# Performance work log

Hardware: AMD Instinct MI355X
Metric: run time of the kernel (lower is better)

## Reference

```python
import jax, jax.numpy as jnp
import numpy as np

B, C, H, W = 8, 512, 32, 32
N = H * W
FG_THRES, BG_THRES, TOPK = 0.7, 0.6, 12


def setup_inputs() -> dict:
    key = jax.random.key(0)
    k1, k2, k3 = jax.random.split(key, 3)
    feature_q = jax.random.normal(k1, (B, C, H, W), dtype=jnp.float32)
    support_feat = jax.random.normal(k2, (B, C, H, W), dtype=jnp.float32)
    support_mask = jax.random.randint(k3, (B, H, W), 0, 2).astype(jnp.int32)
    return {"feature_q": feature_q, "support_feat": support_feat, "support_mask": support_mask}


def _masked_avg_pool(feat, mask):
    # feat [B,C,H,W], mask [B,1,H,W]; interpolate to same size is identity
    return jnp.sum(feat * mask, axis=(2, 3)) / (jnp.sum(mask, axis=(2, 3)) + 1e-5)


def _cosine(a, b):
    # F.cosine_similarity along channel dim 1 (eps=1e-8), with broadcasting
    dot = jnp.sum(a * b, axis=1)
    na = jnp.sqrt(jnp.sum(a * a, axis=1))
    nb = jnp.sqrt(jnp.sum(b * b, axis=1))
    return dot / jnp.maximum(na * nb, 1e-8)


def _similarity(feature_q, fg_proto, bg_proto):
    sim_fg = _cosine(feature_q, fg_proto)
    sim_bg = _cosine(feature_q, bg_proto)
    return jnp.stack([sim_bg, sim_fg], axis=1) * 10.0  # [B,2,H,W]


def _select_weights(pred, thres):
    # pred [N] -> float {0,1} selection weights; threshold mask, topk-12 fallback
    m = pred > thres
    _, top_idx = jax.lax.top_k(pred, TOPK)
    tm = jnp.zeros_like(m).at[top_idx].set(True)
    return jnp.where(m.sum() > 0, m, tm).astype(pred.dtype)


def _ssp_single(cur_feat, pred_fg, pred_bg):
    # cur_feat [C,N]; masked formulation == torch's variable-length column select
    wf = _select_weights(pred_fg, FG_THRES)
    wb = _select_weights(pred_bg, BG_THRES)
    fg_proto = jnp.sum(cur_feat * wf, axis=-1) / wf.sum()  # [C]
    bg_proto = jnp.sum(cur_feat * wb, axis=-1) / wb.sum()
    cn = cur_feat / jnp.sqrt(jnp.sum(cur_feat * cur_feat, axis=0, keepdims=True))
    sim = (cn.T @ cn) * 2.0  # [N,N] cosine sim, scaled
    neg = jnp.asarray(-1e30, sim.dtype)
    fg_attn = jax.nn.softmax(jnp.where(wf[None, :] > 0, sim, neg), axis=-1)
    bg_attn = jax.nn.softmax(jnp.where(wb[None, :] > 0, sim, neg), axis=-1)
    fg_local = (fg_attn @ cur_feat.T).T  # [C,N]
    bg_local = (bg_attn @ cur_feat.T).T
    return fg_proto, bg_proto, fg_local, bg_local


def reference(feature_q, support_feat, support_mask):
    mask_f = (support_mask == 1).astype(feature_q.dtype)[:, None]  # [B,1,H,W]
    mask_b = (support_mask == 0).astype(feature_q.dtype)[:, None]
    FP = _masked_avg_pool(support_feat, mask_f)[:, :, None, None]  # [B,C,1,1]
    BP = _masked_avg_pool(support_feat, mask_b)[:, :, None, None]
    out_0 = _similarity(feature_q, FP, BP)  # [B,2,H,W]
    pred = jax.nn.softmax(out_0, axis=1).reshape(B, 2, N)
    cur = feature_q.reshape(B, C, N)
    fg_p, bg_p, fg_l, bg_l = jax.vmap(_ssp_single)(cur, pred[:, 1], pred[:, 0])
    SSFP = fg_p[:, :, None, None]
    SSBP = bg_p[:, :, None, None]
    ASBP = bg_l.reshape(B, C, H, W)
    FP_1 = FP * 0.5 + SSFP * 0.5
    BP_1 = SSBP * 0.3 + ASBP * 0.7
    out_1 = _similarity(feature_q, FP_1, BP_1)  # [B,2,H,W]
    return out_1
```

## Files before the change

### kernel.cpp

```cpp
#include <hip/hip_runtime.h>
#include <math.h>

#define Bsz 8
#define Cch 512
#define Npx 1024
#define TOPK 12
#define BN (Bsz * Npx)

typedef __attribute__((ext_vector_type(8))) short bf16x8;
typedef __attribute__((ext_vector_type(4))) float f32x4;

__device__ __forceinline__ unsigned short f2bf(float x) {
    unsigned u = __float_as_uint(x);
    u += 0x7FFF + ((u >> 16) & 1);
    return (unsigned short)(u >> 16);
}
__device__ __forceinline__ float bf2f(unsigned short h) {
    return __uint_as_float(((unsigned)h) << 16);
}

__device__ __forceinline__ float warp_sum64(float v) {
    for (int o = 32; o > 0; o >>= 1) v += __shfl_down(v, o);
    return v;
}
__device__ __forceinline__ float block_sum512(float v, float* s8) {
    v = warp_sum64(v);
    int lane = threadIdx.x & 63, w = threadIdx.x >> 6;
    __syncthreads();
    if (lane == 0) s8[w] = v;
    __syncthreads();
    float r = 0.f;
    #pragma unroll
    for (int k = 0; k < 8; k++) r += s8[k];
    return r;
}

__global__ void k_pool(const float* __restrict__ sf, const int* __restrict__ mask,
                       float* __restrict__ FPo, float* __restrict__ BPo) {
    __shared__ float s4a[4], s4b[4], s4c[4];
    int c = blockIdx.x, b = blockIdx.y, t = threadIdx.x;
    const float4* f4 = (const float4*)(sf + ((size_t)b * Cch + c) * Npx);
    const int4* m4 = (const int4*)(mask + (size_t)b * Npx);
    float4 v = f4[t];
    int4 m = m4[t];
    float sumf = (m.x == 1 ? v.x : 0.f) + (m.y == 1 ? v.y : 0.f)
               + (m.z == 1 ? v.z : 0.f) + (m.w == 1 ? v.w : 0.f);
    float tot = v.x + v.y + v.z + v.w;
    float cf = (float)((m.x == 1) + (m.y == 1) + (m.z == 1) + (m.w == 1));
    sumf = warp_sum64(sumf);
    tot  = warp_sum64(tot);
    cf   = warp_sum64(cf);
    int lane = t & 63, w = t >> 6;
    if (lane == 0) { s4a[w] = sumf; s4b[w] = tot; s4c[w] = cf; }
    __syncthreads();
    if (t == 0) {
        float sA = s4a[0] + s4a[1] + s4a[2] + s4a[3];
        float sB = s4b[0] + s4b[1] + s4b[2] + s4b[3];
        float sC = s4c[0] + s4c[1] + s4c[2] + s4c[3];
        FPo[b * Cch + c] = sA / (sC + 1e-5f);
        BPo[b * Cch + c] = (sB - sA) / ((1024.f - sC) + 1e-5f);
    }
}

__global__ void __launch_bounds__(512) k_predcast(const float* __restrict__ fq,
                       const float* __restrict__ FP, const float* __restrict__ BP,
                       float* __restrict__ dsim, float* __restrict__ invn,
                       unsigned short* __restrict__ Ft) {
    __shared__ float sFP[Cch], sBP[Cch], s8[8];
    __shared__ float rdf[16][32], rdb[16][32], rqq[16][32];
    __shared__ unsigned short S[32][522];
    int b = blockIdx.y, t = threadIdx.x;
    int tx = t & 31, ty = t >> 5;
    int p0 = blockIdx.x * 32;
    int p = p0 + tx;
    sFP[t] = FP[b * Cch + t];
    sBP[t] = BP[b * Cch + t];
    __syncthreads();
    float nf = sqrtf(block_sum512(sFP[t] * sFP[t], s8));
    float nb = sqrtf(block_sum512(sBP[t] * sBP[t], s8));
    const float* q = fq + (size_t)b * Cch * Npx + p;
    float df = 0.f, db = 0.f, qq = 0.f;
    int c0 = ty * 32;
    #pragma unroll 4
    for (int c = 0; c < 32; c += 2) {
        float v0 = q[(size_t)(c0 + c) * Npx];
        float v1 = q[(size_t)(c0 + c + 1) * Npx];
        df += v0 * sFP[c0 + c] + v1 * sFP[c0 + c + 1];
        db += v0 * sBP[c0 + c] + v1 * sBP[c0 + c + 1];
        qq += v0 * v0 + v1 * v1;
        unsigned pk = (unsigned)f2bf(v0) | ((unsigned)f2bf(v1) << 16);
        *(unsigned*)&S[tx][c0 + c] = pk;
    }
    rdf[ty][tx] = df; rdb[ty][tx] = db; rqq[ty][tx] = qq;
    __syncthreads();
    for (int s = 8; s > 0; s >>= 1) {
        if (ty < s) {
            rdf[ty][tx] += rdf[ty + s][tx];
            rdb[ty][tx] += rdb[ty + s][tx];
            rqq[ty][tx] += rqq[ty + s][tx];
        }
        __syncthreads();
    }
    if (ty == 0) {
        float nq = sqrtf(rqq[0][tx]);
        float simf = 10.f * rdf[0][tx] / fmaxf(nq * nf, 1e-8f);
        float simb = 10.f * rdb[0][tx] / fmaxf(nq * nb, 1e-8f);
        dsim[b * Npx + p] = simf - simb;
        invn[b * Npx + p] = 1.f / nq;
    }
    int w = t >> 6, lane = t & 63;
    unsigned short* FtB = Ft + (size_t)b * Npx * Cch;
    for (int pr = w; pr < 32; pr += 8) {
        unsigned* dst = (unsigned*)(FtB + (size_t)(p0 + pr) * Cch);
        #pragma unroll
        for (int it = 0; it < 4; it++) {
            int d = it * 64 + lane;
            dst[d] = *(const unsigned*)&S[pr][d * 2];
        }
    }
}

__global__ void __launch_bounds__(1024) k_selcompact(const float* __restrict__ dsim,
                        const float* __restrict__ invn,
                        const unsigned short* __restrict__ Ft,
                        const float* __restrict__ FP,
                        int* __restrict__ nsf, int* __restrict__ nsb,
                        int* __restrict__ jf, int* __restrict__ jb,
                        float* __restrict__ ivg,
                        float* __restrict__ fgp, float* __restrict__ bgp,
                        float* __restrict__ FP1, float* __restrict__ nfv) {
    __shared__ int wsum[16];
    __shared__ int sns;
    __shared__ float sProto[16][512];
    __shared__ float s16f[16];
    int b = blockIdx.y, t = threadIdx.x;
    int lane = t & 63, w = t >> 6;
    bool isf = (blockIdx.x == 0);
    float d = dsim[b * Npx + t];
    float key = isf ? d : -d;
    float thres = isf ? 0.8472979f : 0.4054651f;
    int flag = (key > thres) ? 1 : 0;
    int x = flag;
    #pragma unroll
    for (int o = 1; o < 64; o <<= 1) {
        int y = __shfl_up(x, o);
        if (lane >= o) x += y;
    }
    if (lane == 63) wsum[w] = x;
    __syncthreads();
    int base = 0, total = 0;
    #pragma unroll
    for (int k = 0; k < 16; k++) {
        int s = wsum[k];
        if (k < w) base += s;
        total += s;
    }
    int* jdst = (isf ? jf : jb) + b * Npx;
    if (total == 0) {
        __shared__ int   sc[Npx];
        __shared__ float v[Npx];
        __shared__ float rv[Npx];
        __shared__ int   ri[Npx];
        v[t] = key; flag = 0;
        __syncthreads();
        for (int k = 0; k < TOPK; k++) {
            rv[t] = v[t]; ri[t] = t;
            __syncthreads();
            for (int s = 512; s > 0; s >>= 1) {
                if (t < s) {
                    float a = rv[t], bb = rv[t + s];
                    int ia = ri[t], ib = ri[t + s];
                    if (bb > a || (bb == a && ib < ia)) { rv[t] = bb; ri[t] = ib; }
                }
                __syncthreads();
            }
            int win = ri[0];
            if (t == win) { flag = 1; v[t] = -INFINITY; }
            __syncthreads();
        }
        sc[t] = flag;
        __syncthreads();
        for (int off = 1; off < 1024; off <<= 1) {
            int xx = (t >= off) ? sc[t - off] : 0;
            __syncthreads();
            sc[t] += xx;
            __syncthreads();
        }
        if (flag) {
            int pos = sc[t] - 1;
            jdst[pos] = t;
            if (!isf) ivg[b * Npx + pos] = invn[b * Npx + t];
        }
        if (t == 1023) sns = sc[1023];
    } else {
        if (flag) {
            int pos = base + x - 1;
            jdst[pos] = t;
            if (!isf) ivg[b * Npx + pos] = invn[b * Npx + t];
        }
        if (t == 0) sns = total;
    }
    __syncthreads();
    int ns = sns;
    if (t == 0) (isf ? nsf : nsb)[b] = ns;
    const unsigned short* FtB = Ft + (size_t)b * Npx * Cch;
    float facc[8] = {0.f, 0.f, 0.f, 0.f, 0.f, 0.f, 0.f, 0.f};
    int k = w;
    int row = (k < ns) ? jdst[k] : 0;
    while (k < ns) {
        int kn = k + 16;
        int rown = (kn < ns) ? jdst[kn] : 0;
        bf16x8 vv = *(const bf16x8*)&FtB[(size_t)row * Cch + lane * 8];
        #pragma unroll
        for (int e = 0; e < 8; e++) facc[e] += bf2f((unsigned short)vv[e]);
        k = kn; row = rown;
    }
    #pragma unroll
    for (int e = 0; e < 8; e++) sProto[w][lane * 8 + e] = facc[e];
    __syncthreads();
    float fp1 = 0.f;
    if (t < 512) {
        float s = 0.f;
        #pragma unroll
        for (int q = 0; q < 16; q++) s += sProto[q][t];
        float pv = s / (float)ns;
        (isf ? fgp : bgp)[b * Cch + t] = pv;
        if (isf) {
            fp1 = 0.5f * FP[b * Cch + t] + 0.5f * pv;
            FP1[b * Cch + t] = fp1;
        }
    }
    if (isf) {
        float v2 = warp_sum64(fp1 * fp1);
        if (lane == 0) s16f[w] = v2;
        __syncthreads();
        if (t == 0) {
            float nn = 0.f;
            #pragma unroll
            for (int q = 0; q < 16; q++) nn += s16f[q];
            nfv[b] = sqrtf(nn);
        }
    }
}

__global__ void __launch_bounds__(512) k_fused(
        const unsigned short* __restrict__ Ft,
        const int* __restrict__ jb, const int* __restrict__ nsb,
        const float* __restrict__ invn, const float* __restrict__ ivg,
        const float* __restrict__ bgp, const float* __restrict__ FP1,
        const float* __restrict__ nfv, float* __restrict__ out) {
    __shared__ unsigned short U[36864];
    __shared__ unsigned short sP[32][1032];
    __shared__ int   sji[1024];
    __shared__ float sfj[1024];
    __shared__ float sfp1full[Cch], sbgfull[Cch];
    __shared__ float sfi[32], sden[32];
    __shared__ float spart[32][3];

    unsigned short (*Bt2)[64][136] = (unsigned short(*)[64][136])U;
    unsigned short (*Vt)[72] = (unsigned short(*)[72])U;

    int bid = blockIdx.x;
    int b = bid & 7;
    int i0 = (bid >> 3) * 32;
    int tid = threadIdx.x;
    int l = tid & 63, w = tid >> 6;
    int ml = l & 15, quad = l >> 4;
    int ns = nsb[b];
    int K64 = ((((ns + 31) & ~31) + 63) & ~63);
    int T = K64 >> 6;

    const unsigned short* FtB = Ft + (size_t)b * Npx * Cch;
    int ig = w & 1, jg = w >> 1;

    bf16x8 afr[4][4];
    {
        const unsigned short* aro = FtB + (size_t)(i0 + ig * 16 + ml) * Cch + quad * 8;
        #pragma unroll
        for (int kt = 0; kt < 4; kt++)
            #pragma unroll
            for (int h = 0; h < 4; h++)
                afr[kt][h] = *(const bf16x8*)(aro + kt * 128 + h * 32);
    }

    for (int j = tid; j < K64; j += 512) {
        sji[j] = (j < ns) ? jb[b * Npx + j] : jb[b * Npx];
        sfj[j] = (j < ns) ? ivg[b * Npx + j] : 0.f;
    }
    sfp1full[tid] = FP1[b * Cch + tid];
    sbgfull[tid]  = 0.3f * bgp[b * Cch + tid];
    if (tid < 32) sfi[tid] = 2.f * invn[b * Npx + i0 + tid];
    __syncthreads();

    int grow = tid >> 4, gk8 = (tid & 15) * 8;
    for (int j0 = 0; j0 < K64; j0 += 64) {
        const unsigned short* pb0 = FtB + (size_t)sji[j0 + grow] * Cch + gk8;
        const unsigned short* pb1 = FtB + (size_t)sji[j0 + 32 + grow] * Cch + gk8;
        uint4 v0 = *(const uint4*)pb0;
        uint4 v1 = *(const uint4*)pb1;
        f32x4 acc = {};
        #pragma unroll
        for (int kt = 0; kt < 4; kt++) {
            int buf = kt & 1;
            *(uint4*)&Bt2[buf][grow][gk8] = v0;
            *(uint4*)&Bt2[buf][32 + grow][gk8] = v1;
            int kn = (kt + 1) * 128;
            if (kn < Cch) {
                v0 = *(const uint4*)(pb0 + kn);
                v1 = *(const uint4*)(pb1 + kn);
            }
            __syncthreads();
            #pragma unroll
            for (int h = 0; h < 4; h++) {
                bf16x8 bf = *(const bf16x8*)&Bt2[buf][jg * 16 + ml][h * 32 + quad * 8];
                acc = __builtin_amdgcn_mfma_f32_16x16x32_bf16(afr[kt][h], bf, acc, 0, 0, 0);
            }
        }
        #pragma unroll
        for (int r = 0; r < 4; r++) {
            int il = ig * 16 + quad * 4 + r;
            int jl = jg * 16 + ml;
            float e = (j0 + jl < ns) ? __expf(acc[r] * sfi[il] * sfj[j0 + jl]) : 0.f;
            sP[il][j0 + jl] = f2bf(e);
        }
    }
    __syncthreads();

    {
        int i = tid >> 4, jj16 = tid & 15;
        float s = 0.f;
        for (int j = jj16; j < K64; j += 16) s += bf2f(sP[i][j]);
        #pragma unroll
        for (int m = 1; m < 16; m <<= 1) s += __shfl_xor(s, m);
        if (jj16 == 0) sden[i] = s;
    }
    if (tid < 96) ((float*)spart)[tid] = 0.f;
    __syncthreads();

    int jp = tid & 31, cgg = tid >> 5;
    f32x4 accp[4][2] = {};
    const unsigned short* rA = FtB + (size_t)sji[2 * jp] * Cch + cgg * 32;
    const unsigned short* rB = FtB + (size_t)sji[2 * jp + 1] * Cch + cgg * 32;
    uint4 a0 = *(const uint4*)rA, a1 = *(const uint4*)(rA + 8);
    uint4 a2 = *(const uint4*)(rA + 16), a3 = *(const uint4*)(rA + 24);
    uint4 b0 = *(const uint4*)rB, b1 = *(const uint4*)(rB + 8);
    uint4 b2 = *(const uint4*)(rB + 16), b3 = *(const uint4*)(rB + 24);
    for (int jt = 0; jt < T; jt++) {
        {
            unsigned ad[16] = {a0.x, a0.y, a0.z, a0.w, a1.x, a1.y, a1.z, a1.w,
                               a2.x, a2.y, a2.z, a2.w, a3.x, a3.y, a3.z, a3.w};
            unsigned bd[16] = {b0.x, b0.y, b0.z, b0.w, b1.x, b1.y, b1.z, b1.w,
                               b2.x, b2.y, b2.z, b2.w, b3.x, b3.y, b3.z, b3.w};
            #pragma unroll
            for (int d = 0; d < 16; d++) {
                int c = cgg * 32 + 2 * d;
                *(unsigned*)&Vt[c][2 * jp]     = (ad[d] & 0xFFFFu) | (bd[d] << 16);
                *(unsigned*)&Vt[c + 1][2 * jp] = (ad[d] >> 16) | (bd[d] & 0xFFFF0000u);
            }
        }
        if (jt + 1 < T) {
            rA = FtB + (size_t)sji[(jt + 1) * 64 + 2 * jp] * Cch + cgg * 32;
            rB = FtB + (size_t)sji[(jt + 1) * 64 + 2 * jp + 1] * Cch + cgg * 32;
            a0 = *(const uint4*)rA; a1 = *(const uint4*)(rA + 8);
            a2 = *(const uint4*)(rA + 16); a3 = *(const uint4*)(rA + 24);
            b0 = *(const uint4*)rB; b1 = *(const uint4*)(rB + 8);
            b2 = *(const uint4*)(rB + 16); b3 = *(const uint4*)(rB + 24);
        }
        __syncthreads();
        int j0 = jt * 64;
        #pragma unroll
        for (int iff = 0; iff < 2; iff++) {
            bf16x8 p0 = *(const bf16x8*)&sP[iff * 16 + ml][j0 + quad * 8];
            bf16x8 p1 = *(const bf16x8*)&sP[iff * 16 + ml][j0 + 32 + quad * 8];
            #pragma unroll
            for (int cf = 0; cf < 4; cf++) {
                bf16x8 v0 = *(const bf16x8*)&Vt[w * 64 + cf * 16 + ml][quad * 8];
                bf16x8 v1 = *(const bf16x8*)&Vt[w * 64 + cf * 16 + ml][32 + quad * 8];
                accp[cf][iff] = __builtin_amdgcn_mfma_f32_16x16x32_bf16(v0, p0, accp[cf][iff], 0, 0, 0);
                accp[cf][iff] = __builtin_amdgcn_mfma_f32_16x16x32_bf16(v1, p1, accp[cf][iff], 0, 0, 0);
            }
        }
        __syncthreads();
    }

    float sdb[2] = {0.f, 0.f}, snb[2] = {0.f, 0.f}, sdf[2] = {0.f, 0.f};
    #pragma unroll
    for (int iff = 0; iff < 2; iff++) {
        int icol = iff * 16 + ml;
        float rdi = 1.f / sden[icol];
        #pragma unroll
        for (int cf = 0; cf < 4; cf++) {
            int clb = w * 64 + cf * 16 + quad * 4;
            const unsigned* qp = (const unsigned*)(FtB + (size_t)(i0 + icol) * Cch + clb);
            unsigned q01 = qp[0], q23 = qp[1];
            float qv[4] = { bf2f((unsigned short)(q01 & 0xFFFFu)),
                            bf2f((unsigned short)(q01 >> 16)),
                            bf2f((unsigned short)(q23 & 0xFFFFu)),
                            bf2f((unsigned short)(q23 >> 16)) };
            #pragma unroll
            for (int r = 0; r < 4; r++) {
                int cl = clb + r;
                float loc = accp[cf][iff][r] * rdi;
                float bp1 = sbgfull[cl] + 0.7f * loc;
                sdb[iff] += qv[r] * bp1;
                snb[iff] += bp1 * bp1;
                sdf[iff] += qv[r] * sfp1full[cl];
            }
        }
    }
    #pragma unroll
    for (int iff = 0; iff < 2; iff++) {
        float a = sdb[iff], bq = snb[iff], c = sdf[iff];
        a += __shfl_xor(a, 16);  a += __shfl_xor(a, 32);
        bq += __shfl_xor(bq, 16); bq += __shfl_xor(bq, 32);
        c += __shfl_xor(c, 16);  c += __shfl_xor(c, 32);
        if (quad == 0) {
            int icol = iff * 16 + ml;
            atomicAdd(&spart[icol][0], a);
            atomicAdd(&spart[icol][1], bq);
            atomicAdd(&spart[icol][2], c);
        }
    }
    __syncthreads();
    if (tid < 32) {
        float db = spart[tid][0], nb = spart[tid][1], df = spart[tid][2];
        float nq = 2.f / sfi[tid];
        float sb2 = 10.f * db / fmaxf(nq * sqrtf(nb), 1e-8f);
        float sf2 = 10.f * df / fmaxf(nq * nfv[b], 1e-8f);
        out[((size_t)b * 2) * Npx + i0 + tid] = sb2;
        out[((size_t)b * 2 + 1) * Npx + i0 + tid] = sf2;
    }
}

extern "C" void kernel_launch(void* const* d_in, const int* in_sizes, int n_in,
                              void* d_out, int out_size, void* d_ws, size_t ws_size,
                              hipStream_t stream) {
    const float* fq = (const float*)d_in[0];
    const float* sf = (const float*)d_in[1];
    const int* mask = (const int*)d_in[2];
    float* out = (float*)d_out;

    float* ws = (float*)d_ws;
    float* FP    = ws;
    float* BP    = FP + Bsz * Cch;
    float* fgp   = BP + Bsz * Cch;
    float* bgp   = fgp + Bsz * Cch;
    float* FP1   = bgp + Bsz * Cch;
    float* nfv   = FP1 + Bsz * Cch;
    float* dsim  = nfv + 8;
    float* invn  = dsim + BN;
    float* ivg   = invn + BN;
    int*   nsf   = (int*)(ivg + BN);
    int*   nsb   = nsf + 8;
    int*   jf    = nsb + 8;
    int*   jb    = jf + BN;
    unsigned short* Ft = (unsigned short*)(jb + BN);

    k_pool<<<dim3(Cch, Bsz), 256, 0, stream>>>(sf, mask, FP, BP);
    k_predcast<<<dim3(Npx / 32, Bsz), 512, 0, stream>>>(fq, FP, BP, dsim, invn, Ft);
    k_selcompact<<<dim3(2, Bsz), 1024, 0, stream>>>(dsim, invn, Ft, FP, nsf, nsb, jf, jb, ivg, fgp, bgp, FP1, nfv);
    k_fused<<<dim3(256), 512, 0, stream>>>(Ft, jb, nsb, invn, ivg, bgp, FP1, nfv, out);
}
```

Before: 123.4 us.

## Chunk key dimension and channel halves to shrink LDS for higher occupancy

Processes the selected background key columns in chunks of 512 and splits the P·V stage into two channel halves. This shrinks shared memory (sP, Vt, sji, sfj) and adds a launch-bounds hint for multiple blocks per CU. The aim is more resident workgroups to hide gather latency, at the cost of extra barriers, re-gathering key rows per channel half, and accumulating the softmax denominator across chunks.

Result: slower. 141.2 us (+14.4%).

```diff
diff --git a/kernel.cpp b/kernel.cpp
--- a/kernel.cpp
+++ b/kernel.cpp
@@ -243,22 +243,22 @@
     }
 }
 
-__global__ void __launch_bounds__(512) k_fused(
+__global__ void __launch_bounds__(512, 4) k_fused(
         const unsigned short* __restrict__ Ft,
         const int* __restrict__ jb, const int* __restrict__ nsb,
         const float* __restrict__ invn, const float* __restrict__ ivg,
         const float* __restrict__ bgp, const float* __restrict__ FP1,
         const float* __restrict__ nfv, float* __restrict__ out) {
-    __shared__ unsigned short U[36864];
-    __shared__ unsigned short sP[32][1032];
-    __shared__ int   sji[1024];
-    __shared__ float sfj[1024];
+    __shared__ unsigned short U[17408];
+    __shared__ unsigned short sP[32][520];
+    __shared__ int   sji[512];
+    __shared__ float sfj[512];
     __shared__ float sfp1full[Cch], sbgfull[Cch];
     __shared__ float sfi[32], sden[32];
     __shared__ float spart[32][3];
 
     unsigned short (*Bt2)[64][136] = (unsigned short(*)[64][136])U;
-    unsigned short (*Vt)[72] = (unsigned short(*)[72])U;
+    unsigned short (*Vt)[68] = (unsigned short(*)[68])U;
 
     int bid = blockIdx.x;
     int b = bid & 7;
@@ -268,7 +268,6 @@
     int ml = l & 15, quad = l >> 4;
     int ns = nsb[b];
     int K64 = ((((ns + 31) & ~31) + 63) & ~63);
-    int T = K64 >> 6;
 
     const unsigned short* FtB = Ft + (size_t)b * Npx * Cch;
     int ig = w & 1, jg = w >> 1;
@@ -283,104 +282,109 @@
                 afr[kt][h] = *(const bf16x8*)(aro + kt * 128 + h * 32);
     }
 
-    for (int j = tid; j < K64; j += 512) {
-        sji[j] = (j < ns) ? jb[b * Npx + j] : jb[b * Npx];
-        sfj[j] = (j < ns) ? ivg[b * Npx + j] : 0.f;
-    }
     sfp1full[tid] = FP1[b * Cch + tid];
     sbgfull[tid]  = 0.3f * bgp[b * Cch + tid];
-    if (tid < 32) sfi[tid] = 2.f * invn[b * Npx + i0 + tid];
-    __syncthreads();
+    if (tid < 32) { sfi[tid] = 2.f * invn[b * Npx + i0 + tid]; sden[tid] = 0.f; }
+    if (tid < 96) ((float*)spart)[tid] = 0.f;
 
     int grow = tid >> 4, gk8 = (tid & 15) * 8;
-    for (int j0 = 0; j0 < K64; j0 += 64) {
-        const unsigned short* pb0 = FtB + (size_t)sji[j0 + grow] * Cch + gk8;
-        const unsigned short* pb1 = FtB + (size_t)sji[j0 + 32 + grow] * Cch + gk8;
-        uint4 v0 = *(const uint4*)pb0;
-        uint4 v1 = *(const uint4*)pb1;
-        f32x4 acc = {};
-        #pragma unroll
-        for (int kt = 0; kt < 4; kt++) {
-            int buf = kt & 1;
-            *(uint4*)&Bt2[buf][grow][gk8] = v0;
-            *(uint4*)&Bt2[buf][32 + grow][gk8] = v1;
-            int kn = (kt + 1) * 128;
-            if (kn < Cch) {
-                v0 = *(const uint4*)(pb0 + kn);
-                v1 = *(const uint4*)(pb1 + kn);
-            }
-            __syncthreads();
-            #pragma unroll
-            for (int h = 0; h < 4; h++) {
-                bf16x8 bf = *(const bf16x8*)&Bt2[buf][jg * 16 + ml][h * 32 + quad * 8];
-                acc = __builtin_amdgcn_mfma_f32_16x16x32_bf16(afr[kt][h], bf, acc, 0, 0, 0);
-            }
-        }
-        #pragma unroll
-        for (int r = 0; r < 4; r++) {
-            int il = ig * 16 + quad * 4 + r;
-            int jl = jg * 16 + ml;
-            float e = (j0 + jl < ns) ? __expf(acc[r] * sfi[il] * sfj[j0 + jl]) : 0.f;
-            sP[il][j0 + jl] = f2bf(e);
-        }
-    }
-    __syncthreads();
-
-    {
-        int i = tid >> 4, jj16 = tid & 15;
-        float s = 0.f;
-        for (int j = jj16; j < K64; j += 16) s += bf2f(sP[i][j]);
-        #pragma unroll
-        for (int m = 1; m < 16; m <<= 1) s += __shfl_xor(s, m);
-        if (jj16 == 0) sden[i] = s;
-    }
-    if (tid < 96) ((float*)spart)[tid] = 0.f;
-    __syncthreads();
-
     int jp = tid & 31, cgg = tid >> 5;
     f32x4 accp[4][2] = {};
-    const unsigned short* rA = FtB + (size_t)sji[2 * jp] * Cch + cgg * 32;
-    const unsigned short* rB = FtB + (size_t)sji[2 * jp + 1] * Cch + cgg * 32;
-    uint4 a0 = *(const uint4*)rA, a1 = *(const uint4*)(rA + 8);
-    uint4 a2 = *(const uint4*)(rA + 16), a3 = *(const uint4*)(rA + 24);
-    uint4 b0 = *(const uint4*)rB, b1 = *(const uint4*)(rB + 8);
-    uint4 b2 = *(const uint4*)(rB + 16), b3 = *(const uint4*)(rB + 24);
-    for (int jt = 0; jt < T; jt++) {
+
+    for (int jh0 = 0; jh0 < K64; jh0 += 512) {
+        int JH = min(512, K64 - jh0);
+        int TH = JH >> 6;
+        __syncthreads();
+        for (int j = tid; j < JH; j += 512) {
+            int gj = jh0 + j;
+            sji[j] = (gj < ns) ? jb[b * Npx + gj] : jb[b * Npx];
+            sfj[j] = (gj < ns) ? ivg[b * Npx + gj] : 0.f;
+        }
+        __syncthreads();
+
+        for (int j0 = 0; j0 < JH; j0 += 64) {
+            const unsigned short* pb0 = FtB + (size_t)sji[j0 + grow] * Cch + gk8;
+            const unsigned short* pb1 = FtB + (size_t)sji[j0 + 32 + grow] * Cch + gk8;
+            uint4 v0 = *(const uint4*)pb0;
+            uint4 v1 = *(const uint4*)pb1;
+            f32x4 acc = {};
+            #pragma unroll
+            for (int kt = 0; kt < 4; kt++) {
+                int buf = kt & 1;
+                *(uint4*)&Bt2[buf][grow][gk8] = v0;
+                *(uint4*)&Bt2[buf][32 + grow][gk8] = v1;
+                int kn = (kt + 1) * 128;
+                if (kn < Cch) {
+                    v0 = *(const uint4*)(pb0 + kn);
+                    v1 = *(const uint4*)(pb1 + kn);
+                }
+                __syncthreads();
+                #pragma unroll
+                for (int h = 0; h < 4; h++) {
+                    bf16x8 bf = *(const bf16x8*)&Bt2[buf][jg * 16 + ml][h * 32 + quad * 8];
+                    acc = __builtin_amdgcn_mfma_f32_16x16x32_bf16(afr[kt][h], bf, acc, 0, 0, 0);
+                }
+            }
+            #pragma unroll
+            for (int r = 0; r < 4; r++) {
+                int il = ig * 16 + quad * 4 + r;
+                int jl = jg * 16 + ml;
+                float e = (jh0 + j0 + jl < ns) ? __expf(acc[r] * sfi[il] * sfj[j0 + jl]) : 0.f;
+                sP[il][j0 + jl] = f2bf(e);
+            }
+        }
+        __syncthreads();
+
         {
-            unsigned ad[16] = {a0.x, a0.y, a0.z, a0.w, a1.x, a1.y, a1.z, a1.w,
-                               a2.x, a2.y, a2.z, a2.w, a3.x, a3.y, a3.z, a3.w};
-            unsigned bd[16] = {b0.x, b0.y, b0.z, b0.w, b1.x, b1.y, b1.z, b1.w,
-                               b2.x, b2.y, b2.z, b2.w, b3.x, b3.y, b3.z, b3.w};
-            #pragma unroll
-            for (int d = 0; d < 16; d++) {
-                int c = cgg * 32 + 2 * d;
-                *(unsigned*)&Vt[c][2 * jp]     = (ad[d] & 0xFFFFu) | (bd[d] << 16);
-                *(unsigned*)&Vt[c + 1][2 * jp] = (ad[d] >> 16) | (bd[d] & 0xFFFF0000u);
+            int i = tid >> 4, jj16 = tid & 15;
+            float s = 0.f;
+            for (int j = jj16; j < JH; j += 16) s += bf2f(sP[i][j]);
+            #pragma unroll
+            for (int m = 1; m < 16; m <<= 1) s += __shfl_xor(s, m);
+            if (jj16 == 0) sden[i] += s;
+        }
+        __syncthreads();
+
+        #pragma unroll
+        for (int ch = 0; ch < 2; ch++) {
+            const unsigned short* rA = FtB + (size_t)sji[2 * jp] * Cch + ch * 256 + cgg * 16;
+            const unsigned short* rB = FtB + (size_t)sji[2 * jp + 1] * Cch + ch * 256 + cgg * 16;
+            uint4 a0 = *(const uint4*)rA, a1 = *(const uint4*)(rA + 8);
+            uint4 b0 = *(const uint4*)rB, b1 = *(const uint4*)(rB + 8);
+            for (int jt = 0; jt < TH; jt++) {
+                {
+                    unsigned av[8] = {a0.x, a0.y, a0.z, a0.w, a1.x, a1.y, a1.z, a1.w};
+                    unsigned bv[8] = {b0.x, b0.y, b0.z, b0.w, b1.x, b1.y, b1.z, b1.w};
+                    #pragma unroll
+                    for (int d = 0; d < 8; d++) {
+                        int c = cgg * 16 + 2 * d;
+                        *(unsigned*)&Vt[c][2 * jp]     = (av[d] & 0xFFFFu) | (bv[d] << 16);
+                        *(unsigned*)&Vt[c + 1][2 * jp] = (av[d] >> 16) | (bv[d] & 0xFFFF0000u);
+                    }
+                }
+                if (jt + 1 < TH) {
+                    rA = FtB + (size_t)sji[(jt + 1) * 64 + 2 * jp] * Cch + ch * 256 + cgg * 16;
+                    rB = FtB + (size_t)sji[(jt + 1) * 64 + 2 * jp + 1] * Cch + ch * 256 + cgg * 16;
+                    a0 = *(const uint4*)rA; a1 = *(const uint4*)(rA + 8);
+                    b0 = *(const uint4*)rB; b1 = *(const uint4*)(rB + 8);
+                }
+                __syncthreads();
+                int j0 = jt * 64;
+                #pragma unroll
+                for (int iff = 0; iff < 2; iff++) {
+                    bf16x8 p0 = *(const bf16x8*)&sP[iff * 16 + ml][j0 + quad * 8];
+                    bf16x8 p1 = *(const bf16x8*)&sP[iff * 16 + ml][j0 + 32 + quad * 8];
+                    #pragma unroll
+                    for (int cf = 0; cf < 2; cf++) {
+                        bf16x8 v0 = *(const bf16x8*)&Vt[w * 32 + cf * 16 + ml][quad * 8];
+                        bf16x8 v1 = *(const bf16x8*)&Vt[w * 32 + cf * 16 + ml][32 + quad * 8];
+                        accp[ch * 2 + cf][iff] = __builtin_amdgcn_mfma_f32_16x16x32_bf16(v0, p0, accp[ch * 2 + cf][iff], 0, 0, 0);
+                        accp[ch * 2 + cf][iff] = __builtin_amdgcn_mfma_f32_16x16x32_bf16(v1, p1, accp[ch * 2 + cf][iff], 0, 0, 0);
+                    }
+                }
+                __syncthreads();
             }
         }
-        if (jt + 1 < T) {
-            rA = FtB + (size_t)sji[(jt + 1) * 64 + 2 * jp] * Cch + cgg * 32;
-            rB = FtB + (size_t)sji[(jt + 1) * 64 + 2 * jp + 1] * Cch + cgg * 32;
-            a0 = *(const uint4*)rA; a1 = *(const uint4*)(rA + 8);
-            a2 = *(const uint4*)(rA + 16); a3 = *(const uint4*)(rA + 24);
-            b0 = *(const uint4*)rB; b1 = *(const uint4*)(rB + 8);
-            b2 = *(const uint4*)(rB + 16); b3 = *(const uint4*)(rB + 24);
-        }
-        __syncthreads();
-        int j0 = jt * 64;
-        #pragma unroll
-        for (int iff = 0; iff < 2; iff++) {
-            bf16x8 p0 = *(const bf16x8*)&sP[iff * 16 + ml][j0 + quad * 8];
-            bf16x8 p1 = *(const bf16x8*)&sP[iff * 16 + ml][j0 + 32 + quad * 8];
-            #pragma unroll
-            for (int cf = 0; cf < 4; cf++) {
-                bf16x8 v0 = *(const bf16x8*)&Vt[w * 64 + cf * 16 + ml][quad * 8];
-                bf16x8 v1 = *(const bf16x8*)&Vt[w * 64 + cf * 16 + ml][32 + quad * 8];
-                accp[cf][iff] = __builtin_amdgcn_mfma_f32_16x16x32_bf16(v0, p0, accp[cf][iff], 0, 0, 0);
-                accp[cf][iff] = __builtin_amdgcn_mfma_f32_16x16x32_bf16(v1, p1, accp[cf][iff], 0, 0, 0);
-            }
-        }
-        __syncthreads();
     }
 
     float sdb[2] = {0.f, 0.f}, snb[2] = {0.f, 0.f}, sdf[2] = {0.f, 0.f};
@@ -389,22 +393,25 @@
         int icol = iff * 16 + ml;
         float rdi = 1.f / sden[icol];
         #pragma unroll
-        for (int cf = 0; cf < 4; cf++) {
-            int clb = w * 64 + cf * 16 + quad * 4;
-            const unsigned* qp = (const unsigned*)(FtB + (size_t)(i0 + icol) * Cch + clb);
-            unsigned q01 = qp[0], q23 = qp[1];
-            float qv[4] = { bf2f((unsigned short)(q01 & 0xFFFFu)),
-                            bf2f((unsigned short)(q01 >> 16)),
-                            bf2f((unsigned short)(q23 & 0xFFFFu)),
-                            bf2f((unsigned short)(q23 >> 16)) };
-            #pragma unroll
-            for (int r = 0; r < 4; r++) {
-                int cl = clb + r;
-                float loc = accp[cf][iff][r] * rdi;
-                float bp1 = sbgfull[cl] + 0.7f * loc;
-                sdb[iff] += qv[r] * bp1;
-                snb[iff] += bp1 * bp1;
-                sdf[iff] += qv[r] * sfp1full[cl];
+        for (int ch = 0; ch < 2; ch++) {
+            #pragma unroll
+            for (int cf = 0; cf < 2; cf++) {
+                int clb = ch * 256 + w * 32 + cf * 16 + quad * 4;
+                const unsigned* qp = (const unsigned*)(FtB + (size_t)(i0 + icol) * Cch + clb);
+                unsigned q01 = qp[0], q23 = qp[1];
+                float qv[4] = { bf2f((unsigned short)(q01 & 0xFFFFu)),
+                                bf2f((unsigned short)(q01 >> 16)),
+                                bf2f((unsigned short)(q23 & 0xFFFFu)),
+                                bf2f((unsigned short)(q23 >> 16)) };
+                #pragma unroll
+                for (int r = 0; r < 4; r++) {
+                    int cl = clb + r;
+                    float loc = accp[ch * 2 + cf][iff][r] * rdi;
+                    float bp1 = sbgfull[cl] + 0.7f * loc;
+                    sdb[iff] += qv[r] * bp1;
+                    snb[iff] += bp1 * bp1;
+                    sdf[iff] += qv[r] * sfp1full[cl];
+                }
             }
         }
     }
```
